# Kernel optimization log

Hardware: AMD Instinct MI355X
Metric: run time of the kernel (lower is better)

Reference implementation:

```python
import jax, jax.numpy as jnp
import numpy as np

NUM_CLASSES = 2
IGNORE_INDEX = 0
B, H, W = 4, 512, 512
BIG_I = 2 ** 30  # int sentinel for 'no seed yet'
INF = jnp.float32(1e9)  # distance when a column/image has no seed


def _edt_to_seed(seed):
    """Exact 2D Euclidean distance transform: distance from every pixel to the
    nearest True pixel in `seed` [H, W] (matches scipy distance_transform_edt
    applied to an image whose zeros are `seed`).
    Pass 1: 1D nearest-seed distance down each column via cummax/cummin scans.
    Pass 2: exact lower envelope across rows by brute-force min over k:
            D^2(i,j) = min_k ( (j-k)^2 + g(i,k)^2 ).
    """
    h, w = seed.shape
    rows = jnp.arange(h, dtype=jnp.int32)[:, None]              # [H,1]
    last = jax.lax.cummax(jnp.where(seed, rows, -1), axis=0)     # last seed above
    d_fwd = jnp.where(last >= 0, rows - last, BIG_I)
    nxt = jax.lax.cummin(jnp.where(seed, rows, BIG_I), axis=0, reverse=True)
    d_bwd = jnp.where(nxt < BIG_I, nxt - rows, BIG_I)
    g = jnp.minimum(d_fwd, d_bwd)                                # [H,W] int
    g2 = jnp.where(g >= BIG_I // 2, INF * INF, (g * g).astype(jnp.float32))
    cols = jnp.arange(w, dtype=jnp.float32)
    sq = (cols[:, None] - cols[None, :]) ** 2                    # [Wj,Wk]
    d2 = jnp.min(g2[:, None, :] + sq[None, :, :], axis=-1)       # [H,Wj]
    return jnp.sqrt(d2)


def _distance_map_one(tgt):
    """tgt: [H, W] int labels -> [num_classes, H, W] signed distance maps."""
    maps = []
    for c in range(NUM_CLASSES):
        if c == IGNORE_INDEX:
            maps.append(jnp.zeros(tgt.shape, jnp.float32))
            continue
        mask = tgt == c
        pos_dist = _edt_to_seed(~mask)   # edt(posmask): dist to nearest background
        neg_dist = _edt_to_seed(mask)    # edt(negmask): dist to nearest foreground
        present = jnp.any(mask)          # 'if mask.sum() > 0' guard
        maps.append(jnp.where(present, neg_dist - pos_dist, 0.0))
    return jnp.stack(maps, axis=0)


def setup_inputs() -> dict:
    key = jax.random.key(0)
    k1, k2 = jax.random.split(key)
    pred = jax.random.normal(k1, (B, NUM_CLASSES, H, W), dtype=jnp.float32)
    target = jax.random.randint(k2, (B, H, W), 0, 2, dtype=jnp.int32)
    return {"pred": pred, "target": target}


def reference(pred, target):
    p = jax.nn.softmax(pred, axis=1)                         # [B,C,H,W]
    # sequential over batch to bound the [H,W,W] EDT intermediate
    dmaps = jax.lax.map(_distance_map_one, target)           # [B,C,H,W]
    return jnp.mean(p * dmaps)
```

## Files before the change

### kernel.cpp

```cpp
#include <hip/hip_runtime.h>
#include <math.h>

#define BB 4
#define HH 512
#define WW 512
#define HWSZ (HH * WW)

#define TCOLS 16
#define TCH   32
#define CROWS 16
#define COLS_BLOCKS (BB * (WW / TCOLS))
#define ROWS_BLOCKS (BB * HH)
#define BIGR 0x100000


__global__ __launch_bounds__(512) void edt_cols_kernel(
    const int* __restrict__ target,
    unsigned int* __restrict__ gpack,
    int* __restrict__ counts)
{
    int blk = blockIdx.x;
    int b = blk >> 5;
    int tile = blk & 31;
    int tid = threadIdx.x;
    int c = tid & (TCOLS - 1);
    int ch = tid >> 4;
    int j = tile * TCOLS + c;
    int r0 = ch * CROWS;

    const int* t = target + b * HWSZ + j;

    unsigned int maskN = 0;
#pragma unroll
    for (int i = 0; i < CROWS; ++i)
        maskN |= (unsigned int)(t[(r0 + i) * WW] == 1) << i;
    unsigned int maskP = maskN ^ 0xFFFFu;

    __shared__ int sLN[TCH][TCOLS], sFN[TCH][TCOLS];
    __shared__ int sLP[TCH][TCOLS], sFP[TCH][TCOLS];
    __shared__ int sBN[TCH][TCOLS], sAN[TCH][TCOLS];
    __shared__ int sBP[TCH][TCOLS], sAP[TCH][TCOLS];
    __shared__ int sCnt;

    sLN[ch][c] = maskN ? (r0 + 31 - __builtin_clz(maskN)) : -1;
    sFN[ch][c] = maskN ? (r0 + __builtin_ctz(maskN))      : BIGR;
    sLP[ch][c] = maskP ? (r0 + 31 - __builtin_clz(maskP)) : -1;
    sFP[ch][c] = maskP ? (r0 + __builtin_ctz(maskP))      : BIGR;

    int cnt = __popc(maskN);
#pragma unroll
    for (int off = 32; off > 0; off >>= 1) cnt += __shfl_down(cnt, off, 64);
    if (tid == 0) sCnt = 0;
    __syncthreads();
    if ((tid & 63) == 0) atomicAdd(&sCnt, cnt);

    int w = tid >> 6, lane = tid & 63;
    int cc = 2 * w + (lane >> 5);
    int c2 = lane & 31;
    int iLN = sLN[c2][cc], iLP = sLP[c2][cc];
    int iFN = sFN[c2][cc], iFP = sFP[c2][cc];
#pragma unroll
    for (int d = 1; d < 32; d <<= 1) {
        int uLN = __shfl_up(iLN, d, 64);
        int uLP = __shfl_up(iLP, d, 64);
        if (c2 >= d) { iLN = max(iLN, uLN); iLP = max(iLP, uLP); }
    }
#pragma unroll
    for (int d = 1; d < 32; d <<= 1) {
        int dFN = __shfl_down(iFN, d, 64);
        int dFP = __shfl_down(iFP, d, 64);
        if (c2 + d < 32) { iFN = min(iFN, dFN); iFP = min(iFP, dFP); }
    }
    int bLN = __shfl_up(iLN, 1, 64);  if (c2 == 0)  bLN = -1;
    int bLP = __shfl_up(iLP, 1, 64);  if (c2 == 0)  bLP = -1;
    int aFN = __shfl_down(iFN, 1, 64); if (c2 == 31) aFN = BIGR;
    int aFP = __shfl_down(iFP, 1, 64); if (c2 == 31) aFP = BIGR;
    sBN[c2][cc] = bLN; sBP[c2][cc] = bLP;
    sAN[c2][cc] = aFN; sAP[c2][cc] = aFP;
    __syncthreads();

    int befN = sBN[ch][c], befP = sBP[ch][c];
    int aftN = sAN[ch][c], aftP = sAP[ch][c];
    unsigned int* gp = gpack + b * HWSZ + j;

#pragma unroll
    for (int i = 0; i < CROWS; ++i) {
        int row = r0 + i;
        unsigned int belowN = maskN << (31 - i);
        unsigned int aboveN = maskN >> i;
        unsigned int dfN = belowN ? (unsigned int)__builtin_clz(belowN)
                                  : (befN >= 0 ? (unsigned int)(row - befN) : 0xFFFFu);
        unsigned int dbN = aboveN ? (unsigned int)__builtin_ctz(aboveN)
                                  : (aftN < BIGR ? (unsigned int)(aftN - row) : 0xFFFFu);
        unsigned int gN = dfN < dbN ? dfN : dbN;
        if (gN > 0xFFFFu) gN = 0xFFFFu;

        unsigned int belowP = maskP << (31 - i);
        unsigned int aboveP = maskP >> i;
        unsigned int dfP = belowP ? (unsigned int)__builtin_clz(belowP)
                                  : (befP >= 0 ? (unsigned int)(row - befP) : 0xFFFFu);
        unsigned int dbP = aboveP ? (unsigned int)__builtin_ctz(aboveP)
                                  : (aftP < BIGR ? (unsigned int)(aftP - row) : 0xFFFFu);
        unsigned int gP = dfP < dbP ? dfP : dbP;
        if (gP > 0xFFFFu) gP = 0xFFFFu;

        gp[row * WW] = gN | (gP << 16);
    }

    if (tid == 0) counts[blk] = sCnt;
}

#define SK(x) ((x) + ((x) >> 5))

__global__ __launch_bounds__(64) void edt_rows_kernel(
    const unsigned int* __restrict__ gpack,
    const float* __restrict__ pred,
    double* __restrict__ partials)
{
    __shared__ float g2n[SK(511) + 1];
    __shared__ float g2p[SK(511) + 1];

    int bi = blockIdx.x;
    int b = bi >> 9;
    int i = bi & (HH - 1);
    int k = threadIdx.x;
    int j0 = 8 * k;

    const float* p0 = pred + (b * 2 + 0) * HWSZ + i * WW + j0;
    const float* p1 = pred + (b * 2 + 1) * HWSZ + i * WW + j0;
    float4 a0 = *(const float4*)(p0);
    float4 a1 = *(const float4*)(p0 + 4);
    float4 c0 = *(const float4*)(p1);
    float4 c1 = *(const float4*)(p1 + 4);

    const unsigned int* gp = gpack + b * HWSZ + i * WW;
    unsigned int pk[8];
#pragma unroll
    for (int t = 0; t < 8; ++t) pk[t] = gp[k + 64 * t];
#pragma unroll
    for (int t = 0; t < 8; ++t) {
        int idx = k + 64 * t;
        unsigned int gN = pk[t] & 0xFFFFu;
        unsigned int gP = pk[t] >> 16;
        g2n[SK(idx)] = (gN == 0xFFFFu) ? 1e18f : (float)(gN * gN);
        g2p[SK(idx)] = (gP == 0xFFFFu) ? 1e18f : (float)(gP * gP);
    }
    __syncthreads();

    float bn[8], bp[8];
#pragma unroll
    for (int jj = 0; jj < 8; ++jj) {
        bn[jj] = g2n[SK(j0 + jj)];
        bp[jj] = g2p[SK(j0 + jj)];
    }
    for (int r = 1; r < WW; ++r) {
        float sq = (float)(r * r);
        float mx = 0.0f;
#pragma unroll
        for (int jj = 0; jj < 8; ++jj) mx = fmaxf(mx, fmaxf(bn[jj], bp[jj]));
        if (sq >= mx) break;
#pragma unroll
        for (int jj = 0; jj < 8; ++jj) {
            int kl = j0 + jj - r; kl = kl < 0 ? 0 : kl;
            int kr = j0 + jj + r; kr = kr > (WW - 1) ? (WW - 1) : kr;
            int skl = SK(kl), skr = SK(kr);
            bn[jj] = fminf(bn[jj], sq + g2n[skl]);
            bp[jj] = fminf(bp[jj], sq + g2p[skl]);
            bn[jj] = fminf(bn[jj], sq + g2n[skr]);
            bp[jj] = fminf(bp[jj], sq + g2p[skr]);
        }
    }

    float x0[8] = {a0.x, a0.y, a0.z, a0.w, a1.x, a1.y, a1.z, a1.w};
    float x1[8] = {c0.x, c0.y, c0.z, c0.w, c1.x, c1.y, c1.z, c1.w};
    float acc = 0.0f;
#pragma unroll
    for (int jj = 0; jj < 8; ++jj) {
        float dist = sqrtf(bn[jj]) - sqrtf(bp[jj]);
        float prob = 1.0f / (1.0f + __expf(x0[jj] - x1[jj]));
        acc += prob * dist;
    }
#pragma unroll
    for (int off = 32; off > 0; off >>= 1) acc += __shfl_down(acc, off, 64);
    if (k == 0) partials[bi] = (double)acc;
}

__global__ __launch_bounds__(256) void finalize_kernel(
    const int* __restrict__ counts,
    const double* __restrict__ partials,
    float* __restrict__ out)
{
    __shared__ double red[256];
    __shared__ int pres[BB];
    int tid = threadIdx.x;

    if (tid < BB) pres[tid] = 0;
    __syncthreads();
    if (tid < COLS_BLOCKS && counts[tid] > 0)
        atomicOr(&pres[tid >> 5], 1);
    __syncthreads();

    double s = 0.0;
    for (int idx = tid; idx < ROWS_BLOCKS; idx += 256)
        s += pres[idx >> 9] ? partials[idx] : 0.0;
    red[tid] = s;
    __syncthreads();
    for (int off = 128; off > 0; off >>= 1) {
        if (tid < off) red[tid] += red[tid + off];
        __syncthreads();
    }
    if (tid == 0)
        out[0] = (float)(red[0] * (1.0 / 2097152.0));
}

extern "C" void kernel_launch(void* const* d_in, const int* in_sizes, int n_in,
                              void* d_out, int out_size, void* d_ws, size_t ws_size,
                              hipStream_t stream) {
    const float* pred = (const float*)d_in[0];
    const int* target = (const int*)d_in[1];
    float* out = (float*)d_out;

    char* ws = (char*)d_ws;
    int* counts = (int*)(ws + 0);
    double* partials = (double*)(ws + 1024);
    unsigned int* gpack = (unsigned int*)(ws + 32768);

    edt_cols_kernel<<<COLS_BLOCKS, 512, 0, stream>>>(target, gpack, counts);
    edt_rows_kernel<<<ROWS_BLOCKS, 64, 0, stream>>>(gpack, pred, partials);
    finalize_kernel<<<1, 256, 0, stream>>>(counts, partials, out);
}
```

Before: 75.12 us.

## Drop finalize kernel, accumulate via atomics and vectorize gpack loads

Removes the separate single-block finalize kernel. Each row block now checks per-image presence flags with a wavefront ballot and atomically adds its scaled partial sum into the output, which the column kernel zeroes first. The row kernel also loads the packed column distances as uint4 instead of scalar words. This saves one kernel launch and its serial reduction, but it trades double-precision ordered summation for float atomics that are non-deterministic and less precise.

Result: slower. 95.09 us (+26.6%).

```diff
diff --git a/kernel.cpp b/kernel.cpp
--- a/kernel.cpp
+++ b/kernel.cpp
@@ -17,7 +17,8 @@
 __global__ __launch_bounds__(512) void edt_cols_kernel(
     const int* __restrict__ target,
     unsigned int* __restrict__ gpack,
-    int* __restrict__ counts)
+    int* __restrict__ flags,
+    float* __restrict__ out)
 {
     int blk = blockIdx.x;
     int b = blk >> 5;
@@ -27,6 +28,8 @@
     int ch = tid >> 4;
     int j = tile * TCOLS + c;
     int r0 = ch * CROWS;
+
+    if (blk == 0 && tid == 0) out[0] = 0.0f;
 
     const int* t = target + b * HWSZ + j;
 
@@ -107,7 +110,7 @@
         gp[row * WW] = gN | (gP << 16);
     }
 
-    if (tid == 0) counts[blk] = sCnt;
+    if (tid == 0) flags[blk] = (sCnt > 0);
 }
 
 #define SK(x) ((x) + ((x) >> 5))
@@ -115,7 +118,8 @@
 __global__ __launch_bounds__(64) void edt_rows_kernel(
     const unsigned int* __restrict__ gpack,
     const float* __restrict__ pred,
-    double* __restrict__ partials)
+    const int* __restrict__ flags,
+    float* __restrict__ out)
 {
     __shared__ float g2n[SK(511) + 1];
     __shared__ float g2p[SK(511) + 1];
@@ -125,6 +129,9 @@
     int i = bi & (HH - 1);
     int k = threadIdx.x;
     int j0 = 8 * k;
+
+    int f = flags[(b << 5) + (k & 31)];
+    unsigned long long pres = __ballot(f != 0);
 
     const float* p0 = pred + (b * 2 + 0) * HWSZ + i * WW + j0;
     const float* p1 = pred + (b * 2 + 1) * HWSZ + i * WW + j0;
@@ -133,17 +140,22 @@
     float4 c0 = *(const float4*)(p1);
     float4 c1 = *(const float4*)(p1 + 4);
 
-    const unsigned int* gp = gpack + b * HWSZ + i * WW;
-    unsigned int pk[8];
-#pragma unroll
-    for (int t = 0; t < 8; ++t) pk[t] = gp[k + 64 * t];
-#pragma unroll
-    for (int t = 0; t < 8; ++t) {
-        int idx = k + 64 * t;
-        unsigned int gN = pk[t] & 0xFFFFu;
-        unsigned int gP = pk[t] >> 16;
+    const uint4* gp4 = (const uint4*)(gpack + b * HWSZ + i * WW);
+    uint4 ga = gp4[k];
+    uint4 gb = gp4[k + 64];
+
+    unsigned int va[4] = {ga.x, ga.y, ga.z, ga.w};
+    unsigned int vb[4] = {gb.x, gb.y, gb.z, gb.w};
+#pragma unroll
+    for (int t = 0; t < 4; ++t) {
+        int idx = 4 * k + t;
+        unsigned int gN = va[t] & 0xFFFFu, gP = va[t] >> 16;
         g2n[SK(idx)] = (gN == 0xFFFFu) ? 1e18f : (float)(gN * gN);
         g2p[SK(idx)] = (gP == 0xFFFFu) ? 1e18f : (float)(gP * gP);
+        int idx2 = 256 + 4 * k + t;
+        gN = vb[t] & 0xFFFFu; gP = vb[t] >> 16;
+        g2n[SK(idx2)] = (gN == 0xFFFFu) ? 1e18f : (float)(gN * gN);
+        g2p[SK(idx2)] = (gP == 0xFFFFu) ? 1e18f : (float)(gP * gP);
     }
     __syncthreads();
 
@@ -182,35 +194,9 @@
     }
 #pragma unroll
     for (int off = 32; off > 0; off >>= 1) acc += __shfl_down(acc, off, 64);
-    if (k == 0) partials[bi] = (double)acc;
-}
-
-__global__ __launch_bounds__(256) void finalize_kernel(
-    const int* __restrict__ counts,
-    const double* __restrict__ partials,
-    float* __restrict__ out)
-{
-    __shared__ double red[256];
-    __shared__ int pres[BB];
-    int tid = threadIdx.x;
-
-    if (tid < BB) pres[tid] = 0;
-    __syncthreads();
-    if (tid < COLS_BLOCKS && counts[tid] > 0)
-        atomicOr(&pres[tid >> 5], 1);
-    __syncthreads();
-
-    double s = 0.0;
-    for (int idx = tid; idx < ROWS_BLOCKS; idx += 256)
-        s += pres[idx >> 9] ? partials[idx] : 0.0;
-    red[tid] = s;
-    __syncthreads();
-    for (int off = 128; off > 0; off >>= 1) {
-        if (tid < off) red[tid] += red[tid + off];
-        __syncthreads();
-    }
-    if (tid == 0)
-        out[0] = (float)(red[0] * (1.0 / 2097152.0));
+
+    if (k == 0 && pres)
+        atomicAdd(out, acc * (1.0f / 2097152.0f));
 }
 
 extern "C" void kernel_launch(void* const* d_in, const int* in_sizes, int n_in,
@@ -221,11 +207,9 @@
     float* out = (float*)d_out;
 
     char* ws = (char*)d_ws;
-    int* counts = (int*)(ws + 0);
-    double* partials = (double*)(ws + 1024);
+    int* flags = (int*)(ws + 0);
     unsigned int* gpack = (unsigned int*)(ws + 32768);
 
-    edt_cols_kernel<<<COLS_BLOCKS, 512, 0, stream>>>(target, gpack, counts);
-    edt_rows_kernel<<<ROWS_BLOCKS, 64, 0, stream>>>(gpack, pred, partials);
-    finalize_kernel<<<1, 256, 0, stream>>>(counts, partials, out);
+    edt_cols_kernel<<<COLS_BLOCKS, 512, 0, stream>>>(target, gpack, flags, out);
+    edt_rows_kernel<<<ROWS_BLOCKS, 64, 0, stream>>>(gpack, pred, flags, out);
 }
```
